# Optimization experiments

Hardware: AMD Instinct MI355X
Metric: run time of the kernel (lower is better)

## Reference

```python
import jax, jax.numpy as jnp
import numpy as np


def sparsemax(z):
    # sparsemax along the last axis (matches tfa.activations.sparsemax default axis=-1)
    K = z.shape[-1]
    zs = -jnp.sort(-z, axis=-1)                      # descending sort
    cs = jnp.cumsum(zs, axis=-1)
    k = jnp.arange(1, K + 1, dtype=z.dtype)
    support = 1.0 + k * zs > cs                      # support set indicator
    kmax = jnp.sum(support, axis=-1, keepdims=True)  # |support|, int
    cs_k = jnp.take_along_axis(cs, kmax - 1, axis=-1)
    tau = (cs_k - 1.0) / kmax.astype(z.dtype)
    return jnp.maximum(z - tau, 0.0)


def binary_lut(depth):
    # (depth, 2**depth, 2) table mapping leaf index -> per-level bit / complement
    idx = np.arange(2 ** depth)
    off = 2 ** np.arange(depth)
    bits = (idx[None, :] // off[:, None]) % 2        # (depth, 2**depth)
    return jnp.asarray(np.stack([bits, 1 - bits], axis=-1), dtype=jnp.float32)


def setup_inputs() -> dict:
    key = jax.random.key(0)
    ks = jax.random.split(key, 5)
    B, F, N, D, U = 8192, 256, 128, 6, 16
    return {
        "x": jax.random.normal(ks[0], (B, F), dtype=jnp.float32),
        "feature_selection_logits": jax.random.normal(ks[1], (F, N, D), dtype=jnp.float32),
        "feature_thresholds": jax.random.normal(ks[2], (N, D), dtype=jnp.float32),
        "log_temperatures": jax.random.normal(ks[3], (N, D), dtype=jnp.float32) * 0.1,
        "response": jax.random.normal(ks[4], (N, U, 2 ** D), dtype=jnp.float32),
        "depth": D,
    }


def reference(x, feature_selection_logits, feature_thresholds, log_temperatures, response, depth):
    lut = binary_lut(depth)                                          # (d, 2**d, 2)
    selectors = sparsemax(feature_selection_logits)                  # (i, n, d)
    fv = jnp.einsum('bi,ind->bnd', x, selectors)                     # (b, n, d)
    tl = (fv - feature_thresholds) * jnp.exp(-log_temperatures)      # (b, n, d)
    tl = jnp.stack([-tl, tl], axis=-1)                               # (b, n, d, 2)
    gates = jnp.clip(0.5 * tl + 0.5, 0.0, 1.0)                       # sparsemoid
    rg = jnp.einsum('bnds,dcs->bndc', gates, lut)                    # (b, n, d, 2**d)
    rg = jnp.prod(rg, axis=-2)                                       # (b, n, 2**d)
    resp = jnp.einsum('bnc,nuc->bnu', rg, response)                  # (b, n, u)
    return jnp.mean(resp, axis=1)                                    # (b, u)
```

## Files before the change

kernel.cpp:

```cpp
#include <hip/hip_runtime.h>


typedef float f32x4 __attribute__((ext_vector_type(4)));
typedef unsigned int u32;
typedef _Float16 h16;
typedef _Float16 h16x2 __attribute__((ext_vector_type(2)));
typedef _Float16 h16x8 __attribute__((ext_vector_type(8)));

#define WPF_OFF   0
#define RESPF_OFF 393216
#define BIAS_OFF  655360

union h2u { h16x2 h; u32 u; };
union hbits { h16 h; unsigned short s; };
union fragh { u32 w[4]; h16x8 v; int4 i4; h16x2 h2[4]; };

__device__ inline unsigned short h16r(float f) {
    hbits t; t.h = (h16)f; return t.s;
}
__device__ inline u32 packh2(float a, float b) {
    h2u t; t.h[0] = (h16)a; t.h[1] = (h16)b; return t.u;
}

__device__ inline f32x4 mfma_f16(h16x8 a, h16x8 b, f32x4 c) {
    return __builtin_amdgcn_mfma_f32_16x16x32_f16(a, b, c, 0, 0, 0);
}

__global__ __launch_bounds__(256) void k_prep(const float* __restrict__ fsl,
                                              const float* __restrict__ thr,
                                              const float* __restrict__ logt,
                                              const float* __restrict__ resp,
                                              unsigned short* __restrict__ WpF,
                                              unsigned short* __restrict__ respF,
                                              float* __restrict__ bias) {
    int bb  = blockIdx.x;
    int tid = threadIdx.x;
    if (bb < 128) {
        __shared__ unsigned short sm[8][192];
        int ib = (bb & 31) * 8;
        int nb = (bb >> 5) * 32;
        int il = tid >> 5;
        int nl = tid & 31;
        int i = ib + il;
        int n = nb + nl;
        const float* zp = fsl + (i * 128 + n) * 6;

        float z[6], zs[6];
        #pragma unroll
        for (int d = 0; d < 6; ++d) { z[d] = zp[d]; zs[d] = z[d]; }
        #pragma unroll
        for (int a = 0; a < 5; ++a) {
            #pragma unroll
            for (int b = a + 1; b < 6; ++b) {
                float hi = fmaxf(zs[a], zs[b]);
                float lo = fminf(zs[a], zs[b]);
                zs[a] = hi; zs[b] = lo;
            }
        }
        float cs = 0.f, csel = 0.f;
        int   km = 1;
        #pragma unroll
        for (int k = 0; k < 6; ++k) {
            cs += zs[k];
            if (1.0f + (float)(k + 1) * zs[k] > cs) { km = k + 1; csel = cs; }
        }
        float tau = (csel - 1.0f) / (float)km;

        #pragma unroll
        for (int d = 0; d < 6; ++d) {
            float invT = expf(-logt[n * 6 + d]);
            float sel  = fmaxf(z[d] - tau, 0.0f);
            float wv   = sel * 0.5f * invT;
            sm[il][nl * 6 + d] = h16r(wv);
            if (i == 0) bias[n * 6 + d] = 0.5f - 0.5f * invT * thr[n * 6 + d];
        }
        __syncthreads();

        if (tid < 192) {
            int ct  = (nb * 6) / 16 + (tid >> 4);
            int clm = tid & 15;
            int kt  = ib >> 5;
            int lq  = (ib >> 3) & 3;
            union { unsigned short s[8]; int4 i4; } o;
            #pragma unroll
            for (int j = 0; j < 8; ++j) o.s[j] = sm[j][tid];
            *(int4*)(WpF + (size_t)(((ct * 8 + kt) * 64 + lq * 16 + clm) * 8)) = o.i4;
        }
    } else {
        int t = (bb - 128) * 256 + tid;
        int n  = t >> 7;
        int k2 = (t >> 6) & 1;
        int l  = t & 63;
        int u  = l & 15;
        int c0 = k2 * 32 + (l >> 4) * 8;
        const float* rp = resp + n * 1024 + u * 64 + c0;
        float4 ra = *(const float4*)rp;
        float4 rb = *(const float4*)(rp + 4);
        int4 o;
        o.x = (int)packh2(ra.x, ra.y);
        o.y = (int)packh2(ra.z, ra.w);
        o.z = (int)packh2(rb.x, rb.y);
        o.w = (int)packh2(rb.z, rb.w);
        ((int4*)respF)[(n * 2 + k2) * 64 + l] = o;
    }
}

__global__ __launch_bounds__(1024, 4) void k_main(const float* __restrict__ x,
                                                  const unsigned short* __restrict__ WpF,
                                                  const unsigned short* __restrict__ respF,
                                                  const float* __restrict__ bias,
                                                  float* __restrict__ out) {
    __shared__ char smemraw[65536];
    const int4* xf4 = (const int4*)smemraw;

    int tid = threadIdx.x;
    int w  = tid >> 6;
    int l  = tid & 63;
    int cl = l & 15;
    int lq = l >> 4;
    int rowbase = blockIdx.x * 32;
    int ctbase  = w * 3;

    unsigned short* gw = (unsigned short*)(smemraw + 16384 + w * 3072);

    {
        int k8  = tid & 31;
        int row = tid >> 5;
        const float* xp = x + (size_t)(rowbase + row) * 256 + k8 * 8;
        float4 xa = *(const float4*)(xp);
        float4 xb = *(const float4*)(xp + 4);
        int4 p;
        p.x = (int)packh2(xa.x, xa.y);
        p.y = (int)packh2(xa.z, xa.w);
        p.z = (int)packh2(xb.x, xb.y);
        p.w = (int)packh2(xb.z, xb.w);
        int rt = row >> 4, rl = row & 15, kt = k8 >> 2, klq = k8 & 3;
        char* basep = smemraw + (size_t)(rt * 8 + kt) * 1024
                              + (size_t)(((klq * 16 + rl) ^ kt) * 16);
        *(int4*)basep = p;
    }
    __syncthreads();

    f32x4 acc[3][2];
    #pragma unroll
    for (int j = 0; j < 3; ++j) {
        acc[j][0] = (f32x4){0.f, 0.f, 0.f, 0.f};
        acc[j][1] = (f32x4){0.f, 0.f, 0.f, 0.f};
    }
    const int4* wp4 = (const int4*)WpF;

    #pragma unroll
    for (int kt = 0; kt < 8; ++kt) {
        fragh b[3];
        #pragma unroll
        for (int j = 0; j < 3; ++j)
            b[j].i4 = wp4[((ctbase + j) * 8 + kt) * 64 + l];
        #pragma unroll
        for (int rt = 0; rt < 2; ++rt) {
            fragh ah;
            ah.i4 = xf4[(rt * 8 + kt) * 64 + (l ^ kt)];
            #pragma unroll
            for (int j = 0; j < 3; ++j)
                acc[j][rt] = mfma_f16(ah.v, b[j].v, acc[j][rt]);
        }
    }

    #pragma unroll
    for (int j = 0; j < 3; ++j) {
        int colg = (ctbase + j) * 16 + cl;
        int coll = j * 16 + cl;
        float bv = bias[colg];
        #pragma unroll
        for (int rt = 0; rt < 2; ++rt) {
            #pragma unroll
            for (int r = 0; r < 4; ++r) {
                float g = acc[j][rt][r] + bv;
                g = fminf(fmaxf(g, 0.f), 1.f);
                int row = rt * 16 + lq * 4 + r;
                gw[row * 48 + coll] = h16r(g);
            }
        }
    }

    f32x4 oacc0 = (f32x4){0.f, 0.f, 0.f, 0.f};
    f32x4 oacc1 = (f32x4){0.f, 0.f, 0.f, 0.f};
    const int4* rp4 = (const int4*)respF;
    const h16x2 onev = (h16x2){(h16)1.0f, (h16)1.0f};

    #pragma unroll 2
    for (int t2 = 0; t2 < 8; ++t2) {
        int n = w * 8 + t2;
        fragh rb0, rb1;
        rb0.i4 = rp4[(n * 2 + 0) * 64 + l];
        rb1.i4 = rp4[(n * 2 + 1) * 64 + l];
        #pragma unroll
        for (int rt = 0; rt < 2; ++rt) {
            int row = rt * 16 + cl;
            const u32* gp = (const u32*)((const char*)gw + row * 96 + t2 * 12);
            h2u g01u, g23u, g45u;
            g01u.u = gp[0]; g23u.u = gp[1]; g45u.u = gp[2];
            h16x2 g01 = g01u.h, g23 = g23u.h, g45 = g45u.h;
            h16x2 s01 = onev - g01;
            h16x2 s23 = onev - g23;
            h16x2 s45 = onev - g45;
            h16x2 gs0  = __builtin_shufflevector(g01, s01, 0, 2);
            h16x2 b1g  = __builtin_shufflevector(g01, g01, 1, 1);
            h16x2 b1s  = __builtin_shufflevector(s01, s01, 1, 1);
            h16x2 t01a = gs0 * b1g;
            h16x2 t01b = gs0 * b1s;
            h16x2 g2b  = __builtin_shufflevector(g23, g23, 0, 0);
            h16x2 s2b  = __builtin_shufflevector(s23, s23, 0, 0);
            h16x2 pa01 = t01a * g2b;
            h16x2 pa23 = t01b * g2b;
            h16x2 pa45 = t01a * s2b;
            h16x2 pa67 = t01b * s2b;
            h16 f3  = (lq & 1) ? s23[1] : g23[1];
            h16 f4  = (lq & 2) ? s45[0] : g45[0];
            h16 m34 = f3 * f4;
            h16 pbl = m34 * g45[1];
            h16 pbh = m34 * s45[1];
            h16x2 pblb = (h16x2){pbl, pbl};
            h16x2 pbhb = (h16x2){pbh, pbh};
            fragh fa1, fa2;
            fa1.h2[0] = pa01 * pblb; fa1.h2[1] = pa23 * pblb;
            fa1.h2[2] = pa45 * pblb; fa1.h2[3] = pa67 * pblb;
            fa2.h2[0] = pa01 * pbhb; fa2.h2[1] = pa23 * pbhb;
            fa2.h2[2] = pa45 * pbhb; fa2.h2[3] = pa67 * pbhb;
            if (rt == 0) {
                oacc0 = mfma_f16(fa1.v, rb0.v, oacc0);
                oacc0 = mfma_f16(fa2.v, rb1.v, oacc0);
            } else {
                oacc1 = mfma_f16(fa1.v, rb0.v, oacc1);
                oacc1 = mfma_f16(fa2.v, rb1.v, oacc1);
            }
        }
    }

    {
        float* pw = (float*)(smemraw + 16384 + w * 3072);
        int us = (cl + w) & 15;
        #pragma unroll
        for (int r = 0; r < 4; ++r) {
            pw[(lq * 4 + r) * 16 + us]        = oacc0[r];
            pw[(16 + lq * 4 + r) * 16 + us]   = oacc1[r];
        }
    }
    __syncthreads();

    if (tid < 512) {
        int r = tid >> 4, u = tid & 15;
        const float* pb = (const float*)(smemraw + 16384);
        float s = 0.f;
        #pragma unroll
        for (int ww = 0; ww < 16; ++ww)
            s += pb[ww * 768 + r * 16 + ((u + ww) & 15)];
        out[(size_t)(rowbase + r) * 16 + u] = s * (1.0f / 128.0f);
    }
}

extern "C" void kernel_launch(void* const* d_in, const int* in_sizes, int n_in,
                              void* d_out, int out_size, void* d_ws, size_t ws_size,
                              hipStream_t stream) {
    (void)in_sizes; (void)n_in; (void)out_size; (void)ws_size;
    const float* x    = (const float*)d_in[0];
    const float* fsl  = (const float*)d_in[1];
    const float* thr  = (const float*)d_in[2];
    const float* logt = (const float*)d_in[3];
    const float* resp = (const float*)d_in[4];

    char* ws = (char*)d_ws;
    unsigned short* WpF   = (unsigned short*)(ws + WPF_OFF);
    unsigned short* respF = (unsigned short*)(ws + RESPF_OFF);
    float*          bias  = (float*)(ws + BIAS_OFF);
    float* out = (float*)d_out;

    k_prep<<<192, 256, 0, stream>>>(fsl, thr, logt, resp, WpF, respF, bias);
    k_main<<<256, 1024, 0, stream>>>(x, WpF, respF, bias, out);
}
```

Before: 20.90 us.

## Interleave per-column-tile gate GEMM with tree product MFMA and prefetch weights

The first GEMM is split into three column-tile passes. Each pass's epilogue writes its gates, and the tree-product/response MFMAs for the trees that tile covers run right after it, instead of all gate GEMMs finishing before any response work. The weight fragments for the next column tile are prefetched into registers during the current tile's GEMM, and the first tile is issued before the barrier. This is meant to overlap global weight loads with MFMA and to shorten the critical path, at the cost of more live registers (16 fragments) under a 1024-thread launch bound, which risks spills.

```diff
diff --git a/kernel.cpp b/kernel.cpp
--- a/kernel.cpp
+++ b/kernel.cpp
@@ -6,6 +6,12 @@
 typedef _Float16 h16;
 typedef _Float16 h16x2 __attribute__((ext_vector_type(2)));
 typedef _Float16 h16x8 __attribute__((ext_vector_type(8)));
+
+typedef unsigned short __attribute__((may_alias)) u16a;
+typedef u32            __attribute__((may_alias)) u32a;
+typedef float          __attribute__((may_alias)) f32a;
+
+#define MEMFENCE asm volatile("" ::: "memory")
 
 #define WPF_OFF   0
 #define RESPF_OFF 393216
@@ -105,6 +111,55 @@
     }
 }
 
+__device__ inline void pv_tree(const u16a* gw, const int4* rp4, int n, int t2,
+                               int cl, int lq, f32x4& o0, f32x4& o1) {
+    const h16x2 onev = (h16x2){(h16)1.0f, (h16)1.0f};
+    fragh rb0, rb1;
+    rb0.i4 = rp4[(n * 2 + 0) * 64 + (lq * 16 + cl)];
+    rb1.i4 = rp4[(n * 2 + 1) * 64 + (lq * 16 + cl)];
+    #pragma unroll
+    for (int rt = 0; rt < 2; ++rt) {
+        int row = rt * 16 + cl;
+        const u32a* gp = (const u32a*)((const char*)gw + row * 96 + t2 * 12);
+        h2u g01u, g23u, g45u;
+        g01u.u = gp[0]; g23u.u = gp[1]; g45u.u = gp[2];
+        h16x2 g01 = g01u.h, g23 = g23u.h, g45 = g45u.h;
+        h16x2 s01 = onev - g01;
+        h16x2 s23 = onev - g23;
+        h16x2 s45 = onev - g45;
+        h16x2 gs0  = __builtin_shufflevector(g01, s01, 0, 2);
+        h16x2 b1g  = __builtin_shufflevector(g01, g01, 1, 1);
+        h16x2 b1s  = __builtin_shufflevector(s01, s01, 1, 1);
+        h16x2 t01a = gs0 * b1g;
+        h16x2 t01b = gs0 * b1s;
+        h16x2 g2b  = __builtin_shufflevector(g23, g23, 0, 0);
+        h16x2 s2b  = __builtin_shufflevector(s23, s23, 0, 0);
+        h16x2 pa01 = t01a * g2b;
+        h16x2 pa23 = t01b * g2b;
+        h16x2 pa45 = t01a * s2b;
+        h16x2 pa67 = t01b * s2b;
+        h16 f3  = (lq & 1) ? s23[1] : g23[1];
+        h16 f4  = (lq & 2) ? s45[0] : g45[0];
+        h16 m34 = f3 * f4;
+        h16 pbl = m34 * g45[1];
+        h16 pbh = m34 * s45[1];
+        h16x2 pblb = (h16x2){pbl, pbl};
+        h16x2 pbhb = (h16x2){pbh, pbh};
+        fragh fa1, fa2;
+        fa1.h2[0] = pa01 * pblb; fa1.h2[1] = pa23 * pblb;
+        fa1.h2[2] = pa45 * pblb; fa1.h2[3] = pa67 * pblb;
+        fa2.h2[0] = pa01 * pbhb; fa2.h2[1] = pa23 * pbhb;
+        fa2.h2[2] = pa45 * pbhb; fa2.h2[3] = pa67 * pbhb;
+        if (rt == 0) {
+            o0 = mfma_f16(fa1.v, rb0.v, o0);
+            o0 = mfma_f16(fa2.v, rb1.v, o0);
+        } else {
+            o1 = mfma_f16(fa1.v, rb0.v, o1);
+            o1 = mfma_f16(fa2.v, rb1.v, o1);
+        }
+    }
+}
+
 __global__ __launch_bounds__(1024, 4) void k_main(const float* __restrict__ x,
                                                   const unsigned short* __restrict__ WpF,
                                                   const unsigned short* __restrict__ respF,
@@ -121,7 +176,9 @@
     int rowbase = blockIdx.x * 32;
     int ctbase  = w * 3;
 
-    unsigned short* gw = (unsigned short*)(smemraw + 16384 + w * 3072);
+    u16a* gw = (u16a*)(smemraw + 16384 + w * 3072);
+    const int4* wp4 = (const int4*)WpF;
+    const int4* rp4 = (const int4*)respF;
 
     {
         int k8  = tid & 31;
@@ -139,105 +196,70 @@
                               + (size_t)(((klq * 16 + rl) ^ kt) * 16);
         *(int4*)basep = p;
     }
+
+    fragh Bc[8], Bn[8];
+    #pragma unroll
+    for (int kt = 0; kt < 8; ++kt)
+        Bc[kt].i4 = wp4[((ctbase + 0) * 8 + kt) * 64 + l];
+    MEMFENCE;
+
     __syncthreads();
-
-    f32x4 acc[3][2];
-    #pragma unroll
-    for (int j = 0; j < 3; ++j) {
-        acc[j][0] = (f32x4){0.f, 0.f, 0.f, 0.f};
-        acc[j][1] = (f32x4){0.f, 0.f, 0.f, 0.f};
-    }
-    const int4* wp4 = (const int4*)WpF;
-
-    #pragma unroll
-    for (int kt = 0; kt < 8; ++kt) {
-        fragh b[3];
-        #pragma unroll
-        for (int j = 0; j < 3; ++j)
-            b[j].i4 = wp4[((ctbase + j) * 8 + kt) * 64 + l];
-        #pragma unroll
-        for (int rt = 0; rt < 2; ++rt) {
-            fragh ah;
-            ah.i4 = xf4[(rt * 8 + kt) * 64 + (l ^ kt)];
-            #pragma unroll
-            for (int j = 0; j < 3; ++j)
-                acc[j][rt] = mfma_f16(ah.v, b[j].v, acc[j][rt]);
-        }
-    }
-
-    #pragma unroll
-    for (int j = 0; j < 3; ++j) {
-        int colg = (ctbase + j) * 16 + cl;
-        int coll = j * 16 + cl;
-        float bv = bias[colg];
-        #pragma unroll
-        for (int rt = 0; rt < 2; ++rt) {
-            #pragma unroll
-            for (int r = 0; r < 4; ++r) {
-                float g = acc[j][rt][r] + bv;
-                g = fminf(fmaxf(g, 0.f), 1.f);
-                int row = rt * 16 + lq * 4 + r;
-                gw[row * 48 + coll] = h16r(g);
-            }
-        }
-    }
 
     f32x4 oacc0 = (f32x4){0.f, 0.f, 0.f, 0.f};
     f32x4 oacc1 = (f32x4){0.f, 0.f, 0.f, 0.f};
-    const int4* rp4 = (const int4*)respF;
-    const h16x2 onev = (h16x2){(h16)1.0f, (h16)1.0f};
-
-    #pragma unroll 2
-    for (int t2 = 0; t2 < 8; ++t2) {
-        int n = w * 8 + t2;
-        fragh rb0, rb1;
-        rb0.i4 = rp4[(n * 2 + 0) * 64 + l];
-        rb1.i4 = rp4[(n * 2 + 1) * 64 + l];
-        #pragma unroll
-        for (int rt = 0; rt < 2; ++rt) {
-            int row = rt * 16 + cl;
-            const u32* gp = (const u32*)((const char*)gw + row * 96 + t2 * 12);
-            h2u g01u, g23u, g45u;
-            g01u.u = gp[0]; g23u.u = gp[1]; g45u.u = gp[2];
-            h16x2 g01 = g01u.h, g23 = g23u.h, g45 = g45u.h;
-            h16x2 s01 = onev - g01;
-            h16x2 s23 = onev - g23;
-            h16x2 s45 = onev - g45;
-            h16x2 gs0  = __builtin_shufflevector(g01, s01, 0, 2);
-            h16x2 b1g  = __builtin_shufflevector(g01, g01, 1, 1);
-            h16x2 b1s  = __builtin_shufflevector(s01, s01, 1, 1);
-            h16x2 t01a = gs0 * b1g;
-            h16x2 t01b = gs0 * b1s;
-            h16x2 g2b  = __builtin_shufflevector(g23, g23, 0, 0);
-            h16x2 s2b  = __builtin_shufflevector(s23, s23, 0, 0);
-            h16x2 pa01 = t01a * g2b;
-            h16x2 pa23 = t01b * g2b;
-            h16x2 pa45 = t01a * s2b;
-            h16x2 pa67 = t01b * s2b;
-            h16 f3  = (lq & 1) ? s23[1] : g23[1];
-            h16 f4  = (lq & 2) ? s45[0] : g45[0];
-            h16 m34 = f3 * f4;
-            h16 pbl = m34 * g45[1];
-            h16 pbh = m34 * s45[1];
-            h16x2 pblb = (h16x2){pbl, pbl};
-            h16x2 pbhb = (h16x2){pbh, pbh};
-            fragh fa1, fa2;
-            fa1.h2[0] = pa01 * pblb; fa1.h2[1] = pa23 * pblb;
-            fa1.h2[2] = pa45 * pblb; fa1.h2[3] = pa67 * pblb;
-            fa2.h2[0] = pa01 * pbhb; fa2.h2[1] = pa23 * pbhb;
-            fa2.h2[2] = pa45 * pbhb; fa2.h2[3] = pa67 * pbhb;
-            if (rt == 0) {
-                oacc0 = mfma_f16(fa1.v, rb0.v, oacc0);
-                oacc0 = mfma_f16(fa2.v, rb1.v, oacc0);
-            } else {
-                oacc1 = mfma_f16(fa1.v, rb0.v, oacc1);
-                oacc1 = mfma_f16(fa2.v, rb1.v, oacc1);
-            }
-        }
-    }
+    f32x4 acc0, acc1;
+
+#define GEMM_CT(CT, PREF)                                                   \
+    acc0 = (f32x4){0.f, 0.f, 0.f, 0.f};                                     \
+    acc1 = (f32x4){0.f, 0.f, 0.f, 0.f};                                     \
+    _Pragma("unroll")                                                       \
+    for (int kt = 0; kt < 8; ++kt) {                                        \
+        if (PREF) Bn[kt].i4 = wp4[((ctbase + (CT) + 1) * 8 + kt) * 64 + l]; \
+        fragh a0, a1;                                                       \
+        a0.i4 = xf4[(0 * 8 + kt) * 64 + (l ^ kt)];                          \
+        a1.i4 = xf4[(1 * 8 + kt) * 64 + (l ^ kt)];                          \
+        acc0 = mfma_f16(a0.v, Bc[kt].v, acc0);                              \
+        acc1 = mfma_f16(a1.v, Bc[kt].v, acc1);                              \
+        MEMFENCE;                                                           \
+    }
+
+#define EPI_CT(CT) {                                                        \
+    int colg = (ctbase + (CT)) * 16 + cl;                                   \
+    float bv = bias[colg];                                                  \
+    _Pragma("unroll")                                                       \
+    for (int rt = 0; rt < 2; ++rt) {                                        \
+        f32x4 av = rt ? acc1 : acc0;                                        \
+        _Pragma("unroll")                                                   \
+        for (int r = 0; r < 4; ++r) {                                       \
+            float g = av[r] + bv;                                           \
+            g = fminf(fmaxf(g, 0.f), 1.f);                                  \
+            gw[(rt * 16 + lq * 4 + r) * 48 + (CT) * 16 + cl] = h16r(g);     \
+        }                                                                   \
+    } }
+
+#define SWAPB _Pragma("unroll") for (int kk = 0; kk < 8; ++kk) Bc[kk] = Bn[kk];
+
+    GEMM_CT(0, 1)
+    EPI_CT(0)
+    pv_tree(gw, rp4, w * 8 + 0, 0, cl, lq, oacc0, oacc1);
+    pv_tree(gw, rp4, w * 8 + 1, 1, cl, lq, oacc0, oacc1);
+    SWAPB
+
+    GEMM_CT(1, 1)
+    EPI_CT(1)
+    pv_tree(gw, rp4, w * 8 + 2, 2, cl, lq, oacc0, oacc1);
+    pv_tree(gw, rp4, w * 8 + 3, 3, cl, lq, oacc0, oacc1);
+    pv_tree(gw, rp4, w * 8 + 4, 4, cl, lq, oacc0, oacc1);
+    SWAPB
+
+    GEMM_CT(2, 0)
+    EPI_CT(2)
+    pv_tree(gw, rp4, w * 8 + 5, 5, cl, lq, oacc0, oacc1);
+    pv_tree(gw, rp4, w * 8 + 6, 6, cl, lq, oacc0, oacc1);
+    pv_tree(gw, rp4, w * 8 + 7, 7, cl, lq, oacc0, oacc1);
 
     {
-        float* pw = (float*)(smemraw + 16384 + w * 3072);
+        f32a* pw = (f32a*)(smemraw + 16384 + w * 3072);
         int us = (cl + w) & 15;
         #pragma unroll
         for (int r = 0; r < 4; ++r) {
@@ -249,7 +271,7 @@
 
     if (tid < 512) {
         int r = tid >> 4, u = tid & 15;
-        const float* pb = (const float*)(smemraw + 16384);
+        const f32a* pb = (const f32a*)(smemraw + 16384);
         float s = 0.f;
         #pragma unroll
         for (int ww = 0; ww < 16; ++ww)
```

After: 20.05 us (median of 2 runs). 1.04x faster.

## Split trees across block pairs with 64-row tiles and partial-sum combine kernel

Applied to the files above, without the earlier changes.

Each block now handles 64 rows and half of the trees (512 threads), so every weight tile loaded from global memory is reused across four row tiles instead of two. Per-column-tile GEMM is interleaved with the tree products through a double-buffered gate buffer in LDS. Partial sums from the two tree halves go to a workspace and are added by a new small combine kernel. The gain in weight reuse is paid for with an extra kernel launch, a global round-trip for the partials, and a serial GEMM-then-tree schedule within each wave.

```diff
diff --git a/kernel.cpp b/kernel.cpp
--- a/kernel.cpp
+++ b/kernel.cpp
@@ -7,9 +7,14 @@
 typedef _Float16 h16x2 __attribute__((ext_vector_type(2)));
 typedef _Float16 h16x8 __attribute__((ext_vector_type(8)));
 
+typedef unsigned short __attribute__((may_alias)) u16a;
+typedef u32            __attribute__((may_alias)) u32a;
+typedef float          __attribute__((may_alias)) f32a;
+
 #define WPF_OFF   0
 #define RESPF_OFF 393216
 #define BIAS_OFF  655360
+#define PART_OFF  658432
 
 union h2u { h16x2 h; u32 u; };
 union hbits { h16 h; unsigned short s; };
@@ -105,11 +110,60 @@
     }
 }
 
-__global__ __launch_bounds__(1024, 4) void k_main(const float* __restrict__ x,
-                                                  const unsigned short* __restrict__ WpF,
-                                                  const unsigned short* __restrict__ respF,
-                                                  const float* __restrict__ bias,
-                                                  float* __restrict__ out) {
+__device__ inline void pv_tree64(const char* gwb, const int4* rp4, int n,
+                                 int b0, int i0, int b1, int i1, int b2, int i2,
+                                 int cl, int lq, int l,
+                                 f32x4& o0, f32x4& o1, f32x4& o2, f32x4& o3) {
+    const h16x2 onev = (h16x2){(h16)1.0f, (h16)1.0f};
+    fragh rb0, rb1;
+    rb0.i4 = ((const int4*)rp4)[(n * 2 + 0) * 64 + l];
+    rb1.i4 = ((const int4*)rp4)[(n * 2 + 1) * 64 + l];
+    #pragma unroll
+    for (int rr = 0; rr < 4; ++rr) {
+        int row = rr * 16 + cl;
+        const char* base = gwb + row * 32;
+        h2u g01u, g23u, g45u;
+        g01u.u = *(const u32a*)(base + b0 * 2048 + i0 * 4);
+        g23u.u = *(const u32a*)(base + b1 * 2048 + i1 * 4);
+        g45u.u = *(const u32a*)(base + b2 * 2048 + i2 * 4);
+        h16x2 g01 = g01u.h, g23 = g23u.h, g45 = g45u.h;
+        h16x2 s01 = onev - g01;
+        h16x2 s23 = onev - g23;
+        h16x2 s45 = onev - g45;
+        h16x2 gs0  = __builtin_shufflevector(g01, s01, 0, 2);
+        h16x2 b1g  = __builtin_shufflevector(g01, g01, 1, 1);
+        h16x2 b1s  = __builtin_shufflevector(s01, s01, 1, 1);
+        h16x2 t01a = gs0 * b1g;
+        h16x2 t01b = gs0 * b1s;
+        h16x2 g2b  = __builtin_shufflevector(g23, g23, 0, 0);
+        h16x2 s2b  = __builtin_shufflevector(s23, s23, 0, 0);
+        h16x2 pa01 = t01a * g2b;
+        h16x2 pa23 = t01b * g2b;
+        h16x2 pa45 = t01a * s2b;
+        h16x2 pa67 = t01b * s2b;
+        h16 f3  = (lq & 1) ? s23[1] : g23[1];
+        h16 f4  = (lq & 2) ? s45[0] : g45[0];
+        h16 m34 = f3 * f4;
+        h16 pbl = m34 * g45[1];
+        h16 pbh = m34 * s45[1];
+        h16x2 pblb = (h16x2){pbl, pbl};
+        h16x2 pbhb = (h16x2){pbh, pbh};
+        fragh fa1, fa2;
+        fa1.h2[0] = pa01 * pblb; fa1.h2[1] = pa23 * pblb;
+        fa1.h2[2] = pa45 * pblb; fa1.h2[3] = pa67 * pblb;
+        fa2.h2[0] = pa01 * pbhb; fa2.h2[1] = pa23 * pbhb;
+        fa2.h2[2] = pa45 * pbhb; fa2.h2[3] = pa67 * pbhb;
+        f32x4& o = (rr == 0) ? o0 : (rr == 1) ? o1 : (rr == 2) ? o2 : o3;
+        o = mfma_f16(fa1.v, rb0.v, o);
+        o = mfma_f16(fa2.v, rb1.v, o);
+    }
+}
+
+__global__ __launch_bounds__(512, 2) void k_main(const float* __restrict__ x,
+                                                 const unsigned short* __restrict__ WpF,
+                                                 const unsigned short* __restrict__ respF,
+                                                 const float* __restrict__ bias,
+                                                 float* __restrict__ part) {
     __shared__ char smemraw[65536];
     const int4* xf4 = (const int4*)smemraw;
 
@@ -118,14 +172,20 @@
     int l  = tid & 63;
     int cl = l & 15;
     int lq = l >> 4;
-    int rowbase = blockIdx.x * 32;
-    int ctbase  = w * 3;
-
-    unsigned short* gw = (unsigned short*)(smemraw + 16384 + w * 3072);
-
-    {
-        int k8  = tid & 31;
-        int row = tid >> 5;
+    int th = blockIdx.x & 1;
+    int rowbase = (blockIdx.x >> 1) * 64;
+    int ctbase  = th * 24 + w * 3;
+    int ntree   = th * 64 + w * 8;
+
+    char* gwb = smemraw + 32768 + w * 4096;
+    const int4* wp4 = (const int4*)WpF;
+    const int4* rp4 = (const int4*)respF;
+
+    #pragma unroll
+    for (int it = 0; it < 4; ++it) {
+        int a   = it * 512 + tid;
+        int k8  = a & 31;
+        int row = a >> 5;
         const float* xp = x + (size_t)(rowbase + row) * 256 + k8 * 8;
         float4 xa = *(const float4*)(xp);
         float4 xb = *(const float4*)(xp + 4);
@@ -134,128 +194,99 @@
         p.y = (int)packh2(xa.z, xa.w);
         p.z = (int)packh2(xb.x, xb.y);
         p.w = (int)packh2(xb.z, xb.w);
-        int rt = row >> 4, rl = row & 15, kt = k8 >> 2, klq = k8 & 3;
-        char* basep = smemraw + (size_t)(rt * 8 + kt) * 1024
+        int rr = row >> 4, rl = row & 15, kt = k8 >> 2, klq = k8 & 3;
+        char* basep = smemraw + (size_t)(rr * 8 + kt) * 1024
                               + (size_t)(((klq * 16 + rl) ^ kt) * 16);
         *(int4*)basep = p;
     }
     __syncthreads();
 
-    f32x4 acc[3][2];
+    f32x4 o0 = (f32x4){0.f,0.f,0.f,0.f}, o1 = (f32x4){0.f,0.f,0.f,0.f};
+    f32x4 o2 = (f32x4){0.f,0.f,0.f,0.f}, o3 = (f32x4){0.f,0.f,0.f,0.f};
+    f32x4 acc0, acc1, acc2, acc3;
+    fragh Bc[8];
+
+#define GEMM_CT(CT)                                                          \
+    _Pragma("unroll")                                                        \
+    for (int kt = 0; kt < 8; ++kt)                                           \
+        Bc[kt].i4 = wp4[((ctbase + (CT)) * 8 + kt) * 64 + l];                \
+    acc0 = (f32x4){0.f,0.f,0.f,0.f}; acc1 = (f32x4){0.f,0.f,0.f,0.f};        \
+    acc2 = (f32x4){0.f,0.f,0.f,0.f}; acc3 = (f32x4){0.f,0.f,0.f,0.f};        \
+    _Pragma("unroll")                                                        \
+    for (int kt = 0; kt < 8; ++kt) {                                         \
+        fragh a0, a1, a2, a3;                                                \
+        a0.i4 = xf4[(0 * 8 + kt) * 64 + (l ^ kt)];                           \
+        a1.i4 = xf4[(1 * 8 + kt) * 64 + (l ^ kt)];                           \
+        a2.i4 = xf4[(2 * 8 + kt) * 64 + (l ^ kt)];                           \
+        a3.i4 = xf4[(3 * 8 + kt) * 64 + (l ^ kt)];                           \
+        acc0 = mfma_f16(a0.v, Bc[kt].v, acc0);                               \
+        acc1 = mfma_f16(a1.v, Bc[kt].v, acc1);                               \
+        acc2 = mfma_f16(a2.v, Bc[kt].v, acc2);                               \
+        acc3 = mfma_f16(a3.v, Bc[kt].v, acc3);                               \
+    }
+
+#define EPI_CT(CT) {                                                         \
+    float bv = bias[(ctbase + (CT)) * 16 + cl];                              \
+    u16a* gwp = (u16a*)(gwb + ((CT) & 1) * 2048);                            \
+    _Pragma("unroll")                                                        \
+    for (int rr = 0; rr < 4; ++rr) {                                         \
+        f32x4 av = (rr == 0) ? acc0 : (rr == 1) ? acc1 : (rr == 2) ? acc2 : acc3; \
+        _Pragma("unroll")                                                    \
+        for (int r = 0; r < 4; ++r) {                                        \
+            float g = av[r] + bv;                                            \
+            g = fminf(fmaxf(g, 0.f), 1.f);                                   \
+            gwp[(rr * 16 + lq * 4 + r) * 16 + cl] = h16r(g);                 \
+        }                                                                    \
+    } }
+
+    GEMM_CT(0) EPI_CT(0)
+    pv_tree64(gwb, rp4, ntree + 0, 0,0, 0,1, 0,2, cl, lq, l, o0,o1,o2,o3);
+    pv_tree64(gwb, rp4, ntree + 1, 0,3, 0,4, 0,5, cl, lq, l, o0,o1,o2,o3);
+
+    GEMM_CT(1) EPI_CT(1)
+    pv_tree64(gwb, rp4, ntree + 2, 0,6, 0,7, 1,0, cl, lq, l, o0,o1,o2,o3);
+    pv_tree64(gwb, rp4, ntree + 3, 1,1, 1,2, 1,3, cl, lq, l, o0,o1,o2,o3);
+    pv_tree64(gwb, rp4, ntree + 4, 1,4, 1,5, 1,6, cl, lq, l, o0,o1,o2,o3);
+
+    GEMM_CT(2) EPI_CT(2)
+    pv_tree64(gwb, rp4, ntree + 5, 1,7, 0,0, 0,1, cl, lq, l, o0,o1,o2,o3);
+    pv_tree64(gwb, rp4, ntree + 6, 0,2, 0,3, 0,4, cl, lq, l, o0,o1,o2,o3);
+    pv_tree64(gwb, rp4, ntree + 7, 0,5, 0,6, 0,7, cl, lq, l, o0,o1,o2,o3);
+
+    {
+        f32a* pw = (f32a*)gwb;
+        int us = (cl + w) & 15;
+        #pragma unroll
+        for (int r = 0; r < 4; ++r) {
+            pw[(0 * 16 + lq * 4 + r) * 16 + us] = o0[r];
+            pw[(1 * 16 + lq * 4 + r) * 16 + us] = o1[r];
+            pw[(2 * 16 + lq * 4 + r) * 16 + us] = o2[r];
+            pw[(3 * 16 + lq * 4 + r) * 16 + us] = o3[r];
+        }
+    }
+    __syncthreads();
+
+    const f32a* pb = (const f32a*)(smemraw + 32768);
     #pragma unroll
-    for (int j = 0; j < 3; ++j) {
-        acc[j][0] = (f32x4){0.f, 0.f, 0.f, 0.f};
-        acc[j][1] = (f32x4){0.f, 0.f, 0.f, 0.f};
-    }
-    const int4* wp4 = (const int4*)WpF;
-
-    #pragma unroll
-    for (int kt = 0; kt < 8; ++kt) {
-        fragh b[3];
-        #pragma unroll
-        for (int j = 0; j < 3; ++j)
-            b[j].i4 = wp4[((ctbase + j) * 8 + kt) * 64 + l];
-        #pragma unroll
-        for (int rt = 0; rt < 2; ++rt) {
-            fragh ah;
-            ah.i4 = xf4[(rt * 8 + kt) * 64 + (l ^ kt)];
-            #pragma unroll
-            for (int j = 0; j < 3; ++j)
-                acc[j][rt] = mfma_f16(ah.v, b[j].v, acc[j][rt]);
-        }
-    }
-
-    #pragma unroll
-    for (int j = 0; j < 3; ++j) {
-        int colg = (ctbase + j) * 16 + cl;
-        int coll = j * 16 + cl;
-        float bv = bias[colg];
-        #pragma unroll
-        for (int rt = 0; rt < 2; ++rt) {
-            #pragma unroll
-            for (int r = 0; r < 4; ++r) {
-                float g = acc[j][rt][r] + bv;
-                g = fminf(fmaxf(g, 0.f), 1.f);
-                int row = rt * 16 + lq * 4 + r;
-                gw[row * 48 + coll] = h16r(g);
-            }
-        }
-    }
-
-    f32x4 oacc0 = (f32x4){0.f, 0.f, 0.f, 0.f};
-    f32x4 oacc1 = (f32x4){0.f, 0.f, 0.f, 0.f};
-    const int4* rp4 = (const int4*)respF;
-    const h16x2 onev = (h16x2){(h16)1.0f, (h16)1.0f};
-
-    #pragma unroll 2
-    for (int t2 = 0; t2 < 8; ++t2) {
-        int n = w * 8 + t2;
-        fragh rb0, rb1;
-        rb0.i4 = rp4[(n * 2 + 0) * 64 + l];
-        rb1.i4 = rp4[(n * 2 + 1) * 64 + l];
-        #pragma unroll
-        for (int rt = 0; rt < 2; ++rt) {
-            int row = rt * 16 + cl;
-            const u32* gp = (const u32*)((const char*)gw + row * 96 + t2 * 12);
-            h2u g01u, g23u, g45u;
-            g01u.u = gp[0]; g23u.u = gp[1]; g45u.u = gp[2];
-            h16x2 g01 = g01u.h, g23 = g23u.h, g45 = g45u.h;
-            h16x2 s01 = onev - g01;
-            h16x2 s23 = onev - g23;
-            h16x2 s45 = onev - g45;
-            h16x2 gs0  = __builtin_shufflevector(g01, s01, 0, 2);
-            h16x2 b1g  = __builtin_shufflevector(g01, g01, 1, 1);
-            h16x2 b1s  = __builtin_shufflevector(s01, s01, 1, 1);
-            h16x2 t01a = gs0 * b1g;
-            h16x2 t01b = gs0 * b1s;
-            h16x2 g2b  = __builtin_shufflevector(g23, g23, 0, 0);
-            h16x2 s2b  = __builtin_shufflevector(s23, s23, 0, 0);
-            h16x2 pa01 = t01a * g2b;
-            h16x2 pa23 = t01b * g2b;
-            h16x2 pa45 = t01a * s2b;
-            h16x2 pa67 = t01b * s2b;
-            h16 f3  = (lq & 1) ? s23[1] : g23[1];
-            h16 f4  = (lq & 2) ? s45[0] : g45[0];
-            h16 m34 = f3 * f4;
-            h16 pbl = m34 * g45[1];
-            h16 pbh = m34 * s45[1];
-            h16x2 pblb = (h16x2){pbl, pbl};
-            h16x2 pbhb = (h16x2){pbh, pbh};
-            fragh fa1, fa2;
-            fa1.h2[0] = pa01 * pblb; fa1.h2[1] = pa23 * pblb;
-            fa1.h2[2] = pa45 * pblb; fa1.h2[3] = pa67 * pblb;
-            fa2.h2[0] = pa01 * pbhb; fa2.h2[1] = pa23 * pbhb;
-            fa2.h2[2] = pa45 * pbhb; fa2.h2[3] = pa67 * pbhb;
-            if (rt == 0) {
-                oacc0 = mfma_f16(fa1.v, rb0.v, oacc0);
-                oacc0 = mfma_f16(fa2.v, rb1.v, oacc0);
-            } else {
-                oacc1 = mfma_f16(fa1.v, rb0.v, oacc1);
-                oacc1 = mfma_f16(fa2.v, rb1.v, oacc1);
-            }
-        }
-    }
-
-    {
-        float* pw = (float*)(smemraw + 16384 + w * 3072);
-        int us = (cl + w) & 15;
-        #pragma unroll
-        for (int r = 0; r < 4; ++r) {
-            pw[(lq * 4 + r) * 16 + us]        = oacc0[r];
-            pw[(16 + lq * 4 + r) * 16 + us]   = oacc1[r];
-        }
-    }
-    __syncthreads();
-
-    if (tid < 512) {
-        int r = tid >> 4, u = tid & 15;
-        const float* pb = (const float*)(smemraw + 16384);
+    for (int o = 0; o < 2; ++o) {
+        int idx2 = o * 512 + tid;
+        int r = idx2 >> 4, u = idx2 & 15;
         float s = 0.f;
         #pragma unroll
-        for (int ww = 0; ww < 16; ++ww)
-            s += pb[ww * 768 + r * 16 + ((u + ww) & 15)];
-        out[(size_t)(rowbase + r) * 16 + u] = s * (1.0f / 128.0f);
-    }
+        for (int ww = 0; ww < 8; ++ww)
+            s += pb[ww * 1024 + r * 16 + ((u + ww) & 15)];
+        part[(size_t)blockIdx.x * 1024 + idx2] = s;
+    }
+}
+
+__global__ __launch_bounds__(512) void k_comb(const float* __restrict__ part,
+                                              float* __restrict__ out) {
+    int idx = blockIdx.x * 512 + threadIdx.x;
+    int rt64  = idx >> 10;
+    int local = idx & 1023;
+    float v = part[(size_t)(2 * rt64) * 1024 + local]
+            + part[(size_t)(2 * rt64 + 1) * 1024 + local];
+    out[idx] = v * (1.0f / 128.0f);
 }
 
 extern "C" void kernel_launch(void* const* d_in, const int* in_sizes, int n_in,
@@ -272,8 +303,10 @@
     unsigned short* WpF   = (unsigned short*)(ws + WPF_OFF);
     unsigned short* respF = (unsigned short*)(ws + RESPF_OFF);
     float*          bias  = (float*)(ws + BIAS_OFF);
+    float*          part  = (float*)(ws + PART_OFF);
     float* out = (float*)d_out;
 
     k_prep<<<192, 256, 0, stream>>>(fsl, thr, logt, resp, WpF, respF, bias);
-    k_main<<<256, 1024, 0, stream>>>(x, WpF, respF, bias, out);
-}
+    k_main<<<256, 512, 0, stream>>>(x, WpF, respF, bias, part);
+    k_comb<<<256, 512, 0, stream>>>(part, out);
+}
```

New measurement: 21.84 us. +4.5%, slower.
